# Performance work log

Measured on AMD Instinct MI355X. Metric: run time of the kernel, lower is better.

Reference implementation:

```python
import jax, jax.numpy as jnp
import numpy as np
from jax import lax

DN = ('NCHW', 'OIHW', 'NCHW')

def conv2d(x, w, b=None, padding='SAME'):
    y = lax.conv_general_dilated(x, w, (1, 1), padding, dimension_numbers=DN)
    if b is not None:
        y = y + b[None, :, None, None]
    return y

def setup_inputs() -> dict:
    key = jax.random.key(0)
    ks = jax.random.split(key, 9)
    B, C, H, W = 8, 256, 64, 64
    s = lambda fan: 1.0 / np.sqrt(fan)
    return {
        'x': jax.random.normal(ks[0], (B, C, H, W), jnp.float32),
        'qkv_w': jax.random.normal(ks[1], (3 * C, C, 1, 1), jnp.float32) * s(C),
        'qkv_b': jnp.zeros((3 * C,), jnp.float32),
        'out_w': jax.random.normal(ks[2], (C, C, 1, 1), jnp.float32) * s(C),
        'out_b': jnp.zeros((C,), jnp.float32),
        'd1_w': jax.random.normal(ks[3], (8, 1, 3, 3), jnp.float32) * s(9),
        'd1_b': jnp.zeros((8,), jnp.float32),
        'd2_w': jax.random.normal(ks[4], (1, 8, 3, 3), jnp.float32) * s(72),
        'd2_b': jnp.zeros((1,), jnp.float32),
    }

def reference(x, qkv_w, qkv_b, out_w, out_b, d1_w, d1_b, d2_w, d2_b):
    B, C, H, W = x.shape
    N = H * W
    # gradient-energy (Laplacian) density proxy
    gray = x.mean(axis=1, keepdims=True)                      # [B,1,H,W]
    lap_k = jnp.array([[0., -1., 0.], [-1., 4., -1.], [0., -1., 0.]],
                      dtype=x.dtype).reshape(1, 1, 3, 3)
    lap = conv2d(gray, lap_k)                                 # [B,1,H,W]
    h = jax.nn.relu(conv2d(jnp.abs(lap), d1_w, d1_b))         # [B,8,H,W]
    density = jax.nn.sigmoid(conv2d(h, d2_w, d2_b))           # [B,1,H,W]
    # qkv via 1x1 conv == channel matmul
    qkv = jnp.einsum('oc,bchw->bohw', qkv_w[:, :, 0, 0], x) + qkv_b[None, :, None, None]
    q, k, v = jnp.split(qkv, 3, axis=1)                       # each [B,C,H,W]
    q = q.reshape(B, C, N).transpose(0, 2, 1)                 # [B,N,C]
    k = k.reshape(B, C, N)                                    # [B,C,N]
    v = v.reshape(B, C, N).transpose(0, 2, 1)                 # [B,N,C]
    attn = jnp.einsum('bnc,bcm->bnm', q, k) * (float(C) ** -0.5)  # [B,Nq,Nk]
    temperature = 1.0 + 2.0 * (1.0 - density.reshape(B, 1, N))    # per-key [B,1,Nk]
    attn = jax.nn.softmax(attn / temperature, axis=-1)
    out = jnp.einsum('bnm,bmc->bnc', attn, v)                 # [B,N,C]
    out = out.transpose(0, 2, 1).reshape(B, C, H, W)
    out = jnp.einsum('oc,bchw->bohw', out_w[:, :, 0, 0], out) + out_b[None, :, None, None]
    return out + x
```

## Files before the change

### kernel.cpp

```cpp
#include <hip/hip_runtime.h>
#include <hip/hip_bf16.h>

typedef __attribute__((ext_vector_type(8))) short s16x8;
typedef __attribute__((ext_vector_type(4))) float f32x4;
typedef __attribute__((ext_vector_type(16))) float f32x16;
typedef __attribute__((ext_vector_type(4))) unsigned short us4;
typedef __attribute__((ext_vector_type(4))) unsigned int u32x4;

#define MFMA16(a,b,c) __builtin_amdgcn_mfma_f32_16x16x32_bf16((a),(b),(c),0,0,0)
#define MFMA32(a,b,c) __builtin_amdgcn_mfma_f32_32x32x16_bf16((a),(b),(c),0,0,0)

__device__ __forceinline__ float b2f(unsigned short u){
  union{unsigned u; float f;} v; v.u = ((unsigned)u)<<16; return v.f;
}
__device__ __forceinline__ unsigned short f2b(float f){
  union{float f; unsigned u;} v; v.f = f;
  unsigned r = v.u + 0x7fffu + ((v.u>>16)&1u);
  return (unsigned short)(r>>16);
}
__device__ __forceinline__ unsigned cvt_pk_bf16(float lo, float hi){
  unsigned r;
  asm volatile("v_cvt_pk_bf16_f32 %0, %1, %2" : "=v"(r) : "v"(lo), "v"(hi));
  return r;
}

__device__ __forceinline__ void gl_lds16(const void* gp, void* lp){
  __builtin_amdgcn_global_load_lds((const __attribute__((address_space(1))) void*)gp,
                                   (__attribute__((address_space(3))) void*)lp, 16, 0, 0);
}

__device__ __forceinline__ void stage_64x256(void* lds, const unsigned short* g, int stride){
  const int t = threadIdx.x, wv = t>>6;
  #pragma unroll
  for (int i=0;i<8;++i){
    int ch = i*256 + t;
    int row = ch>>5, cc = ch&31, sc = cc ^ (row&7);
    gl_lds16((const char*)(g + (size_t)row*stride) + sc*16,
             (char*)lds + (((size_t)i*256 + wv*64)<<4));
  }
}
__device__ __forceinline__ void stage16KB(void* lds, const unsigned short* g){
  const int tid = threadIdx.x;
  #pragma unroll
  for (int i=0;i<2;++i){
    int ch = i*512 + tid;
    gl_lds16((const char*)(g + (size_t)ch*8), (char*)lds + (size_t)ch*16);
  }
}

__global__ void k_cvt(const float* __restrict__ src, unsigned short* __restrict__ dst){
  int i = blockIdx.x*256 + threadIdx.x;
  f32x4 v = *(const f32x4*)(src + (size_t)i*4);
  us4 o;
  #pragma unroll
  for (int r=0;r<4;++r) o[r] = f2b(v[r]);
  *(us4*)(dst + (size_t)i*4) = o;
}

__global__ void k_transpose(const float* __restrict__ xg, unsigned short* __restrict__ Xtg,
                            float* __restrict__ gray4){
  __shared__ unsigned short T[64*68];
  __shared__ float psum[4*64];
  const int nb = blockIdx.x, cb = blockIdx.y, b = blockIdx.z;
  const int n0 = nb*64, c0 = cb*64;
  const int t = threadIdx.x;
  #pragma unroll
  for (int i=0;i<4;++i){
    int idx = i*256 + t;
    int c = idx>>4, k4 = idx&15;
    f32x4 v = *(const f32x4*)(xg + ((size_t)(b*256 + c0 + c))*4096 + n0 + k4*4);
    us4 o;
    #pragma unroll
    for (int r=0;r<4;++r) o[r] = f2b(v[r]);
    *(us4*)&T[c*68 + k4*4] = o;
  }
  __syncthreads();
  #pragma unroll
  for (int i=0;i<2;++i){
    int idx = i*256 + t;
    int n = idx>>3, ck = idx&7;
    unsigned short vv[8];
    #pragma unroll
    for (int j=0;j<8;++j) vv[j] = T[(ck*8+j)*68 + n];
    *(u32x4*)(Xtg + ((size_t)(b*4096 + n0 + n))*256 + c0 + ck*8) = *(const u32x4*)vv;
  }
  {
    int j = t&63, q = t>>6;
    float s = 0.f;
    #pragma unroll
    for (int c16=0;c16<16;++c16) s += b2f(T[(q*16+c16)*68 + j]);
    psum[q*64 + j] = s;
  }
  __syncthreads();
  if (t < 64){
    float s = psum[t] + psum[64+t] + psum[128+t] + psum[192+t];
    gray4[((size_t)(cb*8 + b))*4096 + n0 + t] = s;
  }
}

__global__ __launch_bounds__(256) void k_density(const float* __restrict__ gray4,
    const float* __restrict__ w1, const float* __restrict__ b1,
    const float* __restrict__ w2, const float* __restrict__ b2_,
    float* __restrict__ sc2){
  __shared__ float gf[4096];
  __shared__ float la[4096];
  __shared__ unsigned short hb[8*4096];
  const int b = blockIdx.x, t = threadIdx.x;
  #pragma unroll
  for (int i=0;i<16;++i){
    int px = i*256 + t;
    float s = gray4[(size_t)(0*8+b)*4096 + px] + gray4[(size_t)(1*8+b)*4096 + px]
            + gray4[(size_t)(2*8+b)*4096 + px] + gray4[(size_t)(3*8+b)*4096 + px];
    gf[px] = s * (1.f/256.f);
  }
  __syncthreads();
  #pragma unroll
  for (int i=0;i<16;++i){
    int px = i*256 + t;
    int hh = px>>6, ww = px&63;
    float c = gf[px];
    float up = hh>0  ? gf[px-64] : 0.f;
    float dn = hh<63 ? gf[px+64] : 0.f;
    float lf = ww>0  ? gf[px-1]  : 0.f;
    float rt = ww<63 ? gf[px+1]  : 0.f;
    la[px] = fabsf(4.f*c - up - dn - lf - rt);
  }
  __syncthreads();
  float w1r[72], b1r[8];
  #pragma unroll
  for (int k=0;k<72;++k) w1r[k] = w1[k];
  #pragma unroll
  for (int j=0;j<8;++j) b1r[j] = b1[j];
  #pragma unroll
  for (int i=0;i<16;++i){
    int px = i*256 + t;
    int hh = px>>6, ww = px&63;
    float tap[9];
    #pragma unroll
    for (int dy=-1;dy<=1;++dy)
      #pragma unroll
      for (int dx=-1;dx<=1;++dx){
        int y=hh+dy, x2=ww+dx;
        tap[(dy+1)*3+dx+1] = (y>=0&&y<64&&x2>=0&&x2<64)? la[y*64+x2] : 0.f;
      }
    #pragma unroll
    for (int j=0;j<8;++j){
      float a = b1r[j];
      #pragma unroll
      for (int k=0;k<9;++k) a += w1r[j*9+k]*tap[k];
      hb[j*4096 + px] = f2b(fmaxf(a, 0.f));
    }
  }
  __syncthreads();
  float w2r[72], b20 = b2_[0];
  #pragma unroll
  for (int k=0;k<72;++k) w2r[k] = w2[k];
  #pragma unroll
  for (int i=0;i<16;++i){
    int px = i*256 + t;
    int hh = px>>6, ww = px&63;
    float a = b20;
    #pragma unroll
    for (int j=0;j<8;++j){
      #pragma unroll
      for (int dy=-1;dy<=1;++dy)
        #pragma unroll
        for (int dx=-1;dx<=1;++dx){
          int y=hh+dy, x2=ww+dx;
          if (y>=0&&y<64&&x2>=0&&x2<64) a += w2r[j*9+(dy+1)*3+(dx+1)]*b2f(hb[j*4096 + y*64+x2]);
        }
    }
    float sig = 1.f/(1.f+__expf(-a));
    sc2[(size_t)b*4096 + px] = 0.09016844f/(3.f - 2.f*sig);
  }
}

__global__ __launch_bounds__(256,2) void k_gemm_qkv(const unsigned short* __restrict__ Wg,
    const unsigned short* __restrict__ Xtg, const float* __restrict__ biasg,
    unsigned short* __restrict__ Qo, unsigned short* __restrict__ Ko, unsigned short* __restrict__ Vto){
  __shared__ unsigned short Wl[64*256], Xl[64*256];
  const int nt_ = blockIdx.x, at = blockIdx.y, b = blockIdx.z;
  const int a0 = at*64, n0 = nt_*64;
  stage_64x256(Wl, Wg + (size_t)a0*256, 256);
  stage_64x256(Xl, Xtg + ((size_t)(b*4096 + n0))*256, 256);
  __syncthreads();
  const int t = threadIdx.x, w = t>>6, lane = t&63, lam = lane&15, lg = lane>>4;
  f32x4 zz = {0.f,0.f,0.f,0.f};
  f32x4 acc[4] = {zz,zz,zz,zz};
  #pragma unroll
  for (int u=0;u<8;++u){
    int ar = 16*w + lam;
    s16x8 af = *(const s16x8*)((const char*)Wl + ar*512 + ((64*u+16*lg) ^ ((ar&7)<<4)));
    #pragma unroll
    for (int ct=0;ct<4;++ct){
      int br = 16*ct + lam;
      s16x8 bf = *(const s16x8*)((const char*)Xl + br*512 + ((64*u+16*lg) ^ ((br&7)<<4)));
      acc[ct] = MFMA16(af, bf, acc[ct]);
    }
  }
  const int ob = a0 + 16*w + 4*lg;
  f32x4 bias4 = *(const f32x4*)(biasg + ob);
  #pragma unroll
  for (int ct=0;ct<4;++ct){
    int n = n0 + 16*ct + lam;
    us4 ov;
    #pragma unroll
    for (int r=0;r<4;++r) ov[r] = f2b(acc[ct][r] + bias4[r]);
    if (a0 < 256){
      *(us4*)(Qo + ((size_t)(b*4096 + n))*256 + ob) = ov;
    } else if (a0 < 512){
      int c4 = ob - 256;
      size_t idx = (((size_t)(b*128 + (n>>5))*1024) + (c4>>3)*32 + (n&31))*8 + (c4&7);
      *(us4*)(Ko + idx) = ov;
    } else {
      int c0v = ob - 512;
      size_t base = ((size_t)(b*128 + (n>>5))*1024 + ((n&31)>>3)*256)*8 + (n&7);
      #pragma unroll
      for (int r=0;r<4;++r)
        Vto[base + (size_t)(c0v+r)*8] = ov[r];
    }
  }
}

__global__ __launch_bounds__(512,2) void k_attn(const unsigned short* __restrict__ Qg,
    const unsigned short* __restrict__ Kg, const unsigned short* __restrict__ Vtg,
    const float* __restrict__ Sg, unsigned short* __restrict__ AOt){
  __shared__ __align__(16) char SL[132096];
  unsigned short* Kl = (unsigned short*)SL;
  unsigned short* Vl = (unsigned short*)(SL + 65536);
  float* mlb = (float*)(SL + 131072);
  float* Ob  = (float*)SL;

  const int tid = threadIdx.x, w = tid>>6, lane = tid&63, l31 = lane&31, h = lane>>5;
  const int g = w>>2;
  const int bid = blockIdx.x;
  const int b = bid&7, qt = bid>>3;
  const int qbase = qt*128 + (w&3)*32;

  const unsigned short* KgB = Kg  + (size_t)b*128*8192;
  const unsigned short* VtB = Vtg + (size_t)b*128*8192;
  const float* SgB = Sg + (size_t)b*4096 + g*2048;

  s16x8 qf[16];
  {
    const unsigned short* qp = Qg + ((size_t)(b*4096 + qbase + l31))*256 + 8*h;
    #pragma unroll
    for (int u=0;u<16;++u) qf[u] = *(const s16x8*)(qp + 16*u);
  }
  f32x16 oa[8];
  #pragma unroll
  for (int nb=0;nb<8;++nb)
    #pragma unroll
    for (int i=0;i<16;++i) oa[nb][i]=0.f;
  float m_run = 0.f, l_run = 0.f;

  #define KBUF(bu,gr) (Kl + ((bu)*2+(gr))*8192)
  #define VBUF(bu,gr) (Vl + ((bu)*2+(gr))*8192)

  stage16KB(KBUF(0,0), KgB);
  stage16KB(KBUF(0,1), KgB + (size_t)64*8192);
  stage16KB(VBUF(0,0), VtB);
  stage16KB(VBUF(0,1), VtB + (size_t)64*8192);
  __syncthreads();

  int cur = 0;
  for (int t=0; t<64; ++t){
    if (t < 63){
      stage16KB(KBUF(cur^1,0), KgB + (size_t)(t+1)*8192);
      stage16KB(KBUF(cur^1,1), KgB + (size_t)(64+t+1)*8192);
      stage16KB(VBUF(cur^1,0), VtB + (size_t)(t+1)*8192);
      stage16KB(VBUF(cur^1,1), VtB + (size_t)(64+t+1)*8192);
    }
    const char* Kc = (const char*)KBUF(cur,g);
    const char* Vc = (const char*)VBUF(cur,g);

    f32x4 sv[4];
    {
      const float* Sp = SgB + t*32;
      #pragma unroll
      for (int j=0;j<4;++j) sv[j] = *(const f32x4*)(Sp + 8*j + 4*h);
    }

    f32x16 st;
    #pragma unroll
    for (int i=0;i<16;++i) st[i]=0.f;
    __builtin_amdgcn_s_setprio(1);
    #pragma unroll
    for (int u=0;u<16;++u){
      s16x8 kf = *(const s16x8*)(Kc + (((2*u+h)*32 + l31)<<4));
      st = MFMA32(kf, qf[u], st);
    }
    __builtin_amdgcn_s_setprio(0);

    float pm[16];
    #pragma unroll
    for (int j=0;j<4;++j)
      #pragma unroll
      for (int i=0;i<4;++i) pm[4*j+i] = st[4*j+i]*sv[j][i];

    float pe[16];
    #pragma unroll
    for (int i=0;i<16;++i) pe[i] = exp2f(pm[i] - m_run);

    float mx[8];
    #pragma unroll
    for (int i=0;i<8;++i) mx[i] = fmaxf(pm[i], pm[8+i]);
    #pragma unroll
    for (int i=0;i<4;++i) mx[i] = fmaxf(mx[i], mx[4+i]);
    float tmax = fmaxf(fmaxf(mx[0],mx[1]), fmaxf(mx[2],mx[3]));
    if (__any(tmax > m_run + 11.5415603f)){
      tmax = fmaxf(tmax, __shfl_xor(tmax, 32));
      float mnew = fmaxf(m_run, tmax);
      float fs = exp2f(m_run - mnew);
      m_run = mnew;
      l_run *= fs;
      #pragma unroll
      for (int i=0;i<16;++i) pe[i] *= fs;
      float fr[16];
      #pragma unroll
      for (int r=0;r<16;++r) fr[r] = __shfl(fs, (r&3)+8*(r>>2)+4*h);
      #pragma unroll
      for (int nb=0;nb<8;++nb)
        #pragma unroll
        for (int r=0;r<16;++r) oa[nb][r] *= fr[r];
    }
    {
      float sm[8];
      #pragma unroll
      for (int i=0;i<8;++i) sm[i] = pe[i] + pe[8+i];
      #pragma unroll
      for (int i=0;i<4;++i) sm[i] += sm[4+i];
      float rs = (sm[0]+sm[1])+(sm[2]+sm[3]);
      rs += __shfl_xor(rs, 32);
      l_run += rs;
    }

    unsigned pq[8];
    #pragma unroll
    for (int j=0;j<4;++j){
      pq[2*j]   = cvt_pk_bf16(pe[4*j],   pe[4*j+1]);
      pq[2*j+1] = cvt_pk_bf16(pe[4*j+2], pe[4*j+3]);
    }

    __builtin_amdgcn_s_setprio(1);
    #pragma unroll
    for (int ks=0;ks<2;++ks){
      const int j0 = 2*ks, j1 = 2*ks+1;
      unsigned s0 = h ? pq[2*j0]   : pq[2*j1];
      unsigned s1 = h ? pq[2*j0+1] : pq[2*j1+1];
      unsigned r0 = (unsigned)__shfl_xor((int)s0, 32);
      unsigned r1 = (unsigned)__shfl_xor((int)s1, 32);
      union { unsigned u[4]; s16x8 v; } pa;
      pa.u[0] = h ? r0 : pq[2*j0];
      pa.u[1] = h ? r1 : pq[2*j0+1];
      pa.u[2] = h ? pq[2*j1]   : r0;
      pa.u[3] = h ? pq[2*j1+1] : r1;
      #pragma unroll
      for (int nb=0;nb<8;++nb){
        s16x8 vf = *(const s16x8*)(Vc + (((2*ks+h)*256 + 32*nb + l31)<<4));
        oa[nb] = MFMA32(pa.v, vf, oa[nb]);
      }
    }
    __builtin_amdgcn_s_setprio(0);

    __syncthreads();
    cur ^= 1;
  }

  if (g == 1){
    if (h == 0){
      mlb[((w-4)*32 + l31)*2]   = m_run;
      mlb[((w-4)*32 + l31)*2+1] = l_run;
    }
    float* Ow = Ob + (size_t)(w-4)*32*256;
    #pragma unroll
    for (int nb=0;nb<8;++nb)
      #pragma unroll
      for (int r=0;r<16;++r){
        int qr = (r&3)+8*(r>>2)+4*h;
        Ow[qr*256 + 32*nb + l31] = oa[nb][r];
      }
  }
  __syncthreads();
  if (g == 0){
    const float* Or = Ob + (size_t)w*32*256;
    #pragma unroll
    for (int r=0;r<16;++r){
      int qr = (r&3)+8*(r>>2)+4*h;
      float m0r = __shfl(m_run, qr);
      float l0r = __shfl(l_run, qr);
      float m1r = mlb[(w*32+qr)*2];
      float l1r = mlb[(w*32+qr)*2+1];
      float M = fmaxf(m0r, m1r);
      float a0 = exp2f(m0r - M), a1 = exp2f(m1r - M);
      float inv = 1.f/(l0r*a0 + l1r*a1);
      a0 *= inv; a1 *= inv;
      unsigned short* dst = AOt + ((size_t)(b*4096 + qbase + qr))*256 + l31;
      #pragma unroll
      for (int nb=0;nb<8;++nb){
        float v = oa[nb][r]*a0 + Or[qr*256 + 32*nb + l31]*a1;
        dst[32*nb] = f2b(v);
      }
    }
  }
  #undef KBUF
  #undef VBUF
}

__global__ __launch_bounds__(256,2) void k_gemm_out(const unsigned short* __restrict__ Ag,
    const unsigned short* __restrict__ Bg, const float* __restrict__ biasg,
    const float* __restrict__ xg, float* __restrict__ outg){
  __shared__ unsigned short Al[64*256], Bl[64*256];
  const int at = blockIdx.x, bt = blockIdx.y, b = blockIdx.z;
  const int a0 = at*64, o0 = bt*64;
  stage_64x256(Al, Ag + ((size_t)(b*4096 + a0))*256, 256);
  stage_64x256(Bl, Bg + (size_t)o0*256, 256);
  __syncthreads();
  const int t = threadIdx.x, w = t>>6, lane = t&63, lam = lane&15, lg = lane>>4;
  f32x4 zz = {0.f,0.f,0.f,0.f};
  f32x4 acc[4] = {zz,zz,zz,zz};
  #pragma unroll
  for (int u=0;u<8;++u){
    int ar = 16*w + lam;
    s16x8 af = *(const s16x8*)((const char*)Al + ar*512 + ((64*u+16*lg) ^ ((ar&7)<<4)));
    #pragma unroll
    for (int ct=0;ct<4;++ct){
      int br = 16*ct + lam;
      s16x8 bf = *(const s16x8*)((const char*)Bl + br*512 + ((64*u+16*lg) ^ ((br&7)<<4)));
      acc[ct] = MFMA16(af, bf, acc[ct]);
    }
  }
  #pragma unroll
  for (int ct=0;ct<4;++ct){
    int o = o0 + 16*ct + lam;
    float ob_ = biasg[o];
    size_t base = ((size_t)(b*256 + o))*4096 + a0 + 16*w + 4*lg;
    f32x4 xv = *(const f32x4*)(xg + base);
    f32x4 ov;
    #pragma unroll
    for (int r=0;r<4;++r) ov[r] = acc[ct][r] + ob_ + xv[r];
    *(f32x4*)(outg + base) = ov;
  }
}

extern "C" void kernel_launch(void* const* d_in, const int* in_sizes, int n_in,
                              void* d_out, int out_size, void* d_ws, size_t ws_size,
                              hipStream_t stream){
  const float* x     = (const float*)d_in[0];
  const float* qkv_w = (const float*)d_in[1];
  const float* qkv_b = (const float*)d_in[2];
  const float* out_w = (const float*)d_in[3];
  const float* out_b = (const float*)d_in[4];
  const float* d1_w  = (const float*)d_in[5];
  const float* d1_b  = (const float*)d_in[6];
  const float* d2_w  = (const float*)d_in[7];
  const float* d2_b  = (const float*)d_in[8];
  float* out = (float*)d_out;

  char* p = (char*)d_ws;
  const size_t BIG = (size_t)8*4096*256*2;
  unsigned short* Xt = (unsigned short*)p; p += BIG;
  unsigned short* Q  = (unsigned short*)p; p += BIG;
  unsigned short* K  = (unsigned short*)p; p += BIG;
  unsigned short* Vt = (unsigned short*)p; p += BIG;
  unsigned short* Wq = (unsigned short*)p; p += (size_t)768*256*2;
  unsigned short* Wo = (unsigned short*)p; p += (size_t)256*256*2;
  float* gray4 = (float*)p; p += (size_t)4*8*4096*4;
  float* sc    = (float*)p; p += (size_t)8*4096*4;

  k_cvt      <<<dim3(192),    256, 0, stream>>>(qkv_w, Wq);
  k_cvt      <<<dim3(64),     256, 0, stream>>>(out_w, Wo);
  k_transpose<<<dim3(64,4,8), 256, 0, stream>>>(x, Xt, gray4);
  k_density  <<<dim3(8),      256, 0, stream>>>(gray4, d1_w, d1_b, d2_w, d2_b, sc);
  k_gemm_qkv <<<dim3(64,12,8),256, 0, stream>>>(Wq, Xt, qkv_b, Q, K, Vt);
  k_attn     <<<dim3(256),    512, 0, stream>>>(Q, K, Vt, sc, Xt);
  k_gemm_out <<<dim3(64,4,8), 256, 0, stream>>>(Xt, Wo, out_b, x, out);
}
```

Before: 287.7 us.

## Software-pipeline attention loop: overlap previous tile's PV with current QK MFMAs

The attention main loop is restructured so each iteration runs the QK^T MFMAs for tile t together with the P·V MFMAs for tile t-1. The previous tile's probabilities stay in registers as packed bf16, and V is read from the other double buffer. A final PV step after the loop drains the pipeline. The aim is to hide the softmax and exp latency behind matrix work. The cost is an extra barrier per iteration and prefetch staging that now starts later, leaving less time to hide global load latency.

```diff
diff --git a/kernel.cpp b/kernel.cpp
--- a/kernel.cpp
+++ b/kernel.cpp
@@ -45,6 +45,28 @@
   for (int i=0;i<2;++i){
     int ch = i*512 + tid;
     gl_lds16((const char*)(g + (size_t)ch*8), (char*)lds + (size_t)ch*16);
+  }
+}
+
+__device__ __forceinline__ void pv_step(const unsigned* pqp, int h, int l31,
+                                        const char* Vp, f32x16* oa){
+  #pragma unroll
+  for (int ks=0;ks<2;++ks){
+    const int j0 = 2*ks, j1 = 2*ks+1;
+    unsigned s0 = h ? pqp[2*j0]   : pqp[2*j1];
+    unsigned s1 = h ? pqp[2*j0+1] : pqp[2*j1+1];
+    unsigned r0 = (unsigned)__shfl_xor((int)s0, 32);
+    unsigned r1 = (unsigned)__shfl_xor((int)s1, 32);
+    union { unsigned u[4]; s16x8 v; } pa;
+    pa.u[0] = h ? r0 : pqp[2*j0];
+    pa.u[1] = h ? r1 : pqp[2*j0+1];
+    pa.u[2] = h ? pqp[2*j1]   : r0;
+    pa.u[3] = h ? pqp[2*j1+1] : r1;
+    #pragma unroll
+    for (int nb=0;nb<8;++nb){
+      s16x8 vf = *(const s16x8*)(Vp + (((2*ks+h)*256 + 32*nb + l31)<<4));
+      oa[nb] = MFMA32(pa.v, vf, oa[nb]);
+    }
   }
 }
 
@@ -253,6 +275,7 @@
     #pragma unroll
     for (int i=0;i<16;++i) oa[nb][i]=0.f;
   float m_run = 0.f, l_run = 0.f;
+  unsigned pqp[8];
 
   #define KBUF(bu,gr) (Kl + ((bu)*2+(gr))*8192)
   #define VBUF(bu,gr) (Vl + ((bu)*2+(gr))*8192)
@@ -265,42 +288,39 @@
 
   int cur = 0;
   for (int t=0; t<64; ++t){
+    const char* Kc = (const char*)KBUF(cur,g);
+    const char* Vp = (const char*)VBUF(cur^1,g);
+
+    f32x16 st;
+    #pragma unroll
+    for (int i=0;i<16;++i) st[i]=0.f;
+    __builtin_amdgcn_s_setprio(1);
+    #pragma unroll
+    for (int u=0;u<16;++u){
+      s16x8 kf = *(const s16x8*)(Kc + (((2*u+h)*32 + l31)<<4));
+      st = MFMA32(kf, qf[u], st);
+    }
+    if (t) pv_step(pqp, h, l31, Vp, oa);
+    __builtin_amdgcn_s_setprio(0);
+    __syncthreads();
+
     if (t < 63){
       stage16KB(KBUF(cur^1,0), KgB + (size_t)(t+1)*8192);
       stage16KB(KBUF(cur^1,1), KgB + (size_t)(64+t+1)*8192);
       stage16KB(VBUF(cur^1,0), VtB + (size_t)(t+1)*8192);
       stage16KB(VBUF(cur^1,1), VtB + (size_t)(64+t+1)*8192);
     }
-    const char* Kc = (const char*)KBUF(cur,g);
-    const char* Vc = (const char*)VBUF(cur,g);
-
     f32x4 sv[4];
     {
       const float* Sp = SgB + t*32;
       #pragma unroll
       for (int j=0;j<4;++j) sv[j] = *(const f32x4*)(Sp + 8*j + 4*h);
     }
-
-    f32x16 st;
-    #pragma unroll
-    for (int i=0;i<16;++i) st[i]=0.f;
-    __builtin_amdgcn_s_setprio(1);
-    #pragma unroll
-    for (int u=0;u<16;++u){
-      s16x8 kf = *(const s16x8*)(Kc + (((2*u+h)*32 + l31)<<4));
-      st = MFMA32(kf, qf[u], st);
-    }
-    __builtin_amdgcn_s_setprio(0);
-
     float pm[16];
     #pragma unroll
     for (int j=0;j<4;++j)
       #pragma unroll
       for (int i=0;i<4;++i) pm[4*j+i] = st[4*j+i]*sv[j][i];
-
-    float pe[16];
-    #pragma unroll
-    for (int i=0;i<16;++i) pe[i] = exp2f(pm[i] - m_run);
 
     float mx[8];
     #pragma unroll
@@ -314,8 +334,6 @@
       float fs = exp2f(m_run - mnew);
       m_run = mnew;
       l_run *= fs;
-      #pragma unroll
-      for (int i=0;i<16;++i) pe[i] *= fs;
       float fr[16];
       #pragma unroll
       for (int r=0;r<16;++r) fr[r] = __shfl(fs, (r&3)+8*(r>>2)+4*h);
@@ -324,6 +342,9 @@
         #pragma unroll
         for (int r=0;r<16;++r) oa[nb][r] *= fr[r];
     }
+    float pe[16];
+    #pragma unroll
+    for (int i=0;i<16;++i) pe[i] = exp2f(pm[i] - m_run);
     {
       float sm[8];
       #pragma unroll
@@ -334,38 +355,17 @@
       rs += __shfl_xor(rs, 32);
       l_run += rs;
     }
-
-    unsigned pq[8];
     #pragma unroll
     for (int j=0;j<4;++j){
-      pq[2*j]   = cvt_pk_bf16(pe[4*j],   pe[4*j+1]);
-      pq[2*j+1] = cvt_pk_bf16(pe[4*j+2], pe[4*j+3]);
-    }
-
-    __builtin_amdgcn_s_setprio(1);
-    #pragma unroll
-    for (int ks=0;ks<2;++ks){
-      const int j0 = 2*ks, j1 = 2*ks+1;
-      unsigned s0 = h ? pq[2*j0]   : pq[2*j1];
-      unsigned s1 = h ? pq[2*j0+1] : pq[2*j1+1];
-      unsigned r0 = (unsigned)__shfl_xor((int)s0, 32);
-      unsigned r1 = (unsigned)__shfl_xor((int)s1, 32);
-      union { unsigned u[4]; s16x8 v; } pa;
-      pa.u[0] = h ? r0 : pq[2*j0];
-      pa.u[1] = h ? r1 : pq[2*j0+1];
-      pa.u[2] = h ? pq[2*j1]   : r0;
-      pa.u[3] = h ? pq[2*j1+1] : r1;
-      #pragma unroll
-      for (int nb=0;nb<8;++nb){
-        s16x8 vf = *(const s16x8*)(Vc + (((2*ks+h)*256 + 32*nb + l31)<<4));
-        oa[nb] = MFMA32(pa.v, vf, oa[nb]);
-      }
-    }
-    __builtin_amdgcn_s_setprio(0);
-
+      pqp[2*j]   = cvt_pk_bf16(pe[4*j],   pe[4*j+1]);
+      pqp[2*j+1] = cvt_pk_bf16(pe[4*j+2], pe[4*j+3]);
+    }
     __syncthreads();
     cur ^= 1;
   }
+
+  pv_step(pqp, h, l31, (const char*)VBUF(cur^1,g), oa);
+  __syncthreads();
 
   if (g == 1){
     if (h == 0){
```

After: 299.4 us. +4.1%, slower.
